# Kernel tuning notes

Measured on AMD Instinct MI355X. Metric: run time of the kernel, lower is better.

## Reference

```python
import jax, jax.numpy as jnp
import numpy as np

N_DET, N_MAP, N_PTS, C = 900, 100, 20, 256
IMG_W, IMG_H = 640.0, 480.0


def _grid_sample(feat, gx, gy):
    """Bilinear grid_sample, align_corners=False, zeros padding.
    feat: [C,H,W]; gx,gy: [N] normalized in [-1,1]. Returns [N,C]."""
    Cc, H, W = feat.shape
    x = (gx + 1.0) * (W * 0.5) - 0.5
    y = (gy + 1.0) * (H * 0.5) - 0.5
    x0 = jnp.floor(x); y0 = jnp.floor(y)
    wx1 = x - x0; wx0 = 1.0 - wx1
    wy1 = y - y0; wy0 = 1.0 - wy1

    def gather(xi, yi):
        inb = (xi >= 0) & (xi <= W - 1) & (yi >= 0) & (yi <= H - 1)
        xc = jnp.clip(xi, 0, W - 1).astype(jnp.int32)
        yc = jnp.clip(yi, 0, H - 1).astype(jnp.int32)
        return feat[:, yc, xc] * inb.astype(feat.dtype)  # [C,N]

    out = (gather(x0, y0) * (wx0 * wy0) + gather(x0 + 1, y0) * (wx1 * wy0)
           + gather(x0, y0 + 1) * (wx0 * wy1) + gather(x0 + 1, y0 + 1) * (wx1 * wy1))
    return out.T  # [N,C]


def _project(E, K, homo):
    """E:[6,4,4], K:[6,3,3], homo:[N,4] -> gx,gy,valid each [6,N]."""
    pc = jnp.einsum('cij,nj->cni', E, homo)            # [6,N,4]
    p2d = jnp.einsum('cij,cnj->cni', K, pc[..., :3])   # [6,N,3]
    depth = p2d[..., 2]
    u = p2d[..., 0] / (depth + 1e-6)
    v = p2d[..., 1] / (depth + 1e-6)
    valid = depth > 0.1
    gx = u / IMG_W * 2.0 - 1.0
    gy = v / IMG_H * 2.0 - 1.0
    return gx, gy, valid


def _sample_multiscale(feats, gx, gy, valid):
    """feats: list of [6,C,H,W]; gx,gy,valid: [6,N] -> [6,N,C]."""
    acc = None
    for f in feats:  # fixed 4 FPN levels
        s = jax.vmap(_grid_sample)(f, gx, gy)  # [6,N,C]
        acc = s if acc is None else acc + s
    acc = acc / len(feats)
    return acc * valid[..., None].astype(acc.dtype)


def setup_inputs():
    key = jax.random.key(0)
    ks = jax.random.split(key, 16)
    f = lambda i, shape, s=1.0: jax.random.normal(ks[i], shape, jnp.float32) * s
    p2 = f(0, (6, C, 120, 160))
    p3 = f(1, (6, C, 60, 80))
    p4 = f(2, (6, C, 30, 40))
    p5 = f(3, (6, C, 15, 20))
    K0 = jnp.array([[500.0, 0.0, 320.0], [0.0, 500.0, 240.0], [0.0, 0.0, 1.0]], jnp.float32)
    intrinsics = jnp.tile(K0, (6, 1, 1)) + f(4, (6, 3, 3), 0.5)
    extrinsics = jnp.tile(jnp.eye(4, dtype=jnp.float32), (6, 1, 1)) + f(5, (6, 4, 4), 0.3)
    det_anchors_3d = f(6, (N_DET, 3), 20.0)
    det_anchors_full = f(7, (N_DET, 11))
    map_anchors = f(8, (N_MAP, N_PTS, 2), 20.0)
    s = 1.0 / float(np.sqrt(C))
    return {
        'p2': p2, 'p3': p3, 'p4': p4, 'p5': p5,
        'intrinsics': intrinsics, 'extrinsics': extrinsics,
        'det_anchors_3d': det_anchors_3d, 'det_anchors_full': det_anchors_full,
        'map_anchors': map_anchors,
        'W1d': f(9, (C, C), s), 'b1d': jnp.zeros((C,), jnp.float32),
        'Wcd': f(10, (C, 4), s), 'bcd': jnp.zeros((4,), jnp.float32),
        'Wod': f(11, (C, 11), s), 'bod': jnp.zeros((11,), jnp.float32),
        'W1m': f(12, (C, C), s), 'b1m': jnp.zeros((C,), jnp.float32),
        'Wcm': f(13, (C, 3), s), 'bcm': jnp.zeros((3,), jnp.float32),
        'Wom': f(14, (C, N_PTS * 2), s), 'bom': jnp.zeros((N_PTS * 2,), jnp.float32),
    }


def reference(p2, p3, p4, p5, intrinsics, extrinsics, det_anchors_3d,
              det_anchors_full, map_anchors, W1d, b1d, Wcd, bcd, Wod, bod,
              W1m, b1m, Wcm, bcm, Wom, bom):
    feats = [p2, p3, p4, p5]
    ones_det = jnp.ones((N_DET, 1), det_anchors_3d.dtype)
    homo_det = jnp.concatenate([det_anchors_3d, ones_det], axis=-1)  # [900,4]
    centers = map_anchors.mean(axis=1)  # [100,2]
    homo_map = jnp.concatenate([centers,
                                jnp.zeros((N_MAP, 1), centers.dtype),
                                jnp.ones((N_MAP, 1), centers.dtype)], axis=-1)  # [100,4]

    gxd, gyd, vd = _project(extrinsics, intrinsics, homo_det)
    det_agg = _sample_multiscale(feats, gxd, gyd, vd).sum(0) / 6.0  # [900,256]
    gxm, gym, vm = _project(extrinsics, intrinsics, homo_map)
    map_agg = _sample_multiscale(feats, gxm, gym, vm).sum(0) / 6.0  # [100,256]

    hd = jax.nn.relu(det_agg @ W1d + b1d)
    det_classes = hd @ Wcd + bcd                     # [900,4]
    det_boxes = det_anchors_full + hd @ Wod + bod    # [900,11]
    hm = jax.nn.relu(map_agg @ W1m + b1m)
    map_classes = hm @ Wcm + bcm                     # [100,3]
    map_lines = map_anchors + (hm @ Wom + bom).reshape(N_MAP, N_PTS, 2)
    return det_classes, det_boxes, map_classes, map_lines
```

## Files before the change

kernel.cpp:

```cpp
#include <hip/hip_runtime.h>

#define CDIM 256
#define NDET 900
#define NMAP 100
#define NPTS 20
#define NBLK (NDET + NMAP)

using u16 = unsigned short;

#define U4OFF 7372800
#define U5OFF 9216000
#define ACC6F 4838400
#define C3STR 1228800
#define C4STR 307200
#define C5STR 76800

__device__ __forceinline__ u16 f2bf(float f) {
    union { float f; unsigned int i; } v; v.f = f;
    return (u16)((v.i + 0x7FFFu + ((v.i >> 16) & 1u)) >> 16);
}
__device__ __forceinline__ float bf2f(u16 u) {
    union { unsigned int i; float f; } v; v.i = ((unsigned int)u) << 16; return v.f;
}

__global__ __launch_bounds__(256, 4) void k1_pack_p2(
    const float* __restrict__ p2, const float* __restrict__ p3,
    const float* __restrict__ p4, const float* __restrict__ p5,
    const float* __restrict__ Kin, const float* __restrict__ Ein,
    const float* __restrict__ det3d, const float* __restrict__ mapanch,
    u16* __restrict__ wsb, float* __restrict__ acc6)
{
    const int b = blockIdx.x;
    const int t = threadIdx.x;

    __shared__ float s_tile[64][65];

    if (b < 1800) {
        const int cam = b / 300;
        const int rem = b % 300;
        const int pxT = rem >> 2, chT = rem & 3;
        const int lane = t & 63, wv = t >> 6;
        #pragma unroll
        for (int cc = 0; cc < 16; ++cc) {
            const int chl = wv * 16 + cc;
            s_tile[chl][lane] = p3[(cam * CDIM + chT * 64 + chl) * 4800 + pxT * 64 + lane];
        }
        __syncthreads();
        #pragma unroll
        for (int pp = 0; pp < 16; ++pp) {
            const int pxl = wv * 16 + pp;
            wsb[(cam * 4800 + pxT * 64 + pxl) * CDIM + chT * 64 + lane] = f2bf(s_tile[lane][pxl]);
        }
        return;
    }
    if (b < 1980) {
        const int id = b - 1800;
        const int cam = id / 30, h = id % 30;
        const float4* __restrict__ src = (const float4*)(p4 + ((cam * CDIM + t) * 30 + h) * 40);
        u16* __restrict__ dst = wsb + U4OFF + ((cam * 30 + h) * 40) * CDIM + t;
        #pragma unroll
        for (int w4 = 0; w4 < 10; ++w4) {
            const float4 v = src[w4];
            dst[(w4 * 4 + 0) * CDIM] = f2bf(v.x);
            dst[(w4 * 4 + 1) * CDIM] = f2bf(v.y);
            dst[(w4 * 4 + 2) * CDIM] = f2bf(v.z);
            dst[(w4 * 4 + 3) * CDIM] = f2bf(v.w);
        }
        return;
    }
    if (b < 2070) {
        const int id = b - 1980;
        const int cam = id / 15, h = id % 15;
        const float4* __restrict__ src = (const float4*)(p5 + ((cam * CDIM + t) * 15 + h) * 20);
        u16* __restrict__ dst = wsb + U5OFF + ((cam * 15 + h) * 20) * CDIM + t;
        #pragma unroll
        for (int w4 = 0; w4 < 5; ++w4) {
            const float4 v = src[w4];
            dst[(w4 * 4 + 0) * CDIM] = f2bf(v.x);
            dst[(w4 * 4 + 1) * CDIM] = f2bf(v.y);
            dst[(w4 * 4 + 2) * CDIM] = f2bf(v.z);
            dst[(w4 * 4 + 3) * CDIM] = f2bf(v.w);
        }
        return;
    }

    const int id = b - 2070;
    const int cam = id / 1000;
    const int pt = id % 1000;
    const bool isDet = (pt < NDET);
    const int m = pt - NDET;

    float h0, h1, h2;
    if (isDet) {
        h0 = det3d[pt * 3 + 0];
        h1 = det3d[pt * 3 + 1];
        h2 = det3d[pt * 3 + 2];
    } else {
        float cx = 0.f, cy = 0.f;
        #pragma unroll
        for (int j = 0; j < NPTS; ++j) {
            cx += mapanch[(m * NPTS + j) * 2 + 0];
            cy += mapanch[(m * NPTS + j) * 2 + 1];
        }
        h0 = cx / (float)NPTS; h1 = cy / (float)NPTS; h2 = 0.f;
    }
    float pc[3];
    #pragma unroll
    for (int i = 0; i < 3; ++i) {
        pc[i] = Ein[cam * 16 + i * 4 + 0] * h0
              + Ein[cam * 16 + i * 4 + 1] * h1
              + Ein[cam * 16 + i * 4 + 2] * h2
              + Ein[cam * 16 + i * 4 + 3] * 1.f;
    }
    const float q0 = Kin[cam*9+0]*pc[0] + Kin[cam*9+1]*pc[1] + Kin[cam*9+2]*pc[2];
    const float q1 = Kin[cam*9+3]*pc[0] + Kin[cam*9+4]*pc[1] + Kin[cam*9+5]*pc[2];
    const float q2 = Kin[cam*9+6]*pc[0] + Kin[cam*9+7]*pc[1] + Kin[cam*9+8]*pc[2];
    const float depth = q2;
    const float u = q0 / (depth + 1e-6f);
    const float v = q1 / (depth + 1e-6f);
    const bool valid = (depth > 0.1f);
    const float gx = u / 640.0f * 2.0f - 1.0f;
    const float gy = v / 480.0f * 2.0f - 1.0f;
    const int H = 120, W = 160;
    const float x = (gx + 1.f) * (W * 0.5f) - 0.5f;
    const float y = (gy + 1.f) * (H * 0.5f) - 0.5f;
    const float x0f = floorf(x), y0f = floorf(y);
    const float wx1 = x - x0f, wx0 = 1.f - wx1;
    const float wy1 = y - y0f, wy0 = 1.f - wy1;
    const float x1f = x0f + 1.f, y1f = y0f + 1.f;
    const bool bx0 = (x0f >= 0.f) && (x0f <= (float)(W - 1));
    const bool bx1 = (x1f >= 0.f) && (x1f <= (float)(W - 1));
    const bool by0 = (y0f >= 0.f) && (y0f <= (float)(H - 1));
    const bool by1 = (y1f >= 0.f) && (y1f <= (float)(H - 1));
    const int xc0 = (int)fminf(fmaxf(x0f, 0.f), (float)(W - 1));
    const int xc1 = (int)fminf(fmaxf(x1f, 0.f), (float)(W - 1));
    const int yc0 = (int)fminf(fmaxf(y0f, 0.f), (float)(H - 1));
    const int yc1 = (int)fminf(fmaxf(y1f, 0.f), (float)(H - 1));
    const float w0 = (bx0 && by0) ? wx0 * wy0 : 0.f;
    const float w1 = (bx1 && by0) ? wx1 * wy0 : 0.f;
    const float w2 = (bx0 && by1) ? wx0 * wy1 : 0.f;
    const float w3 = (bx1 && by1) ? wx1 * wy1 : 0.f;

    float res = 0.f;
    if (valid && ((w0 + w1 + w2 + w3) != 0.f)) {
        const int base = cam * CDIM * H * W + t * (H * W);
        const float v0 = p2[base + yc0 * W + xc0];
        const float v1 = p2[base + yc0 * W + xc1];
        const float v2 = p2[base + yc1 * W + xc0];
        const float v3 = p2[base + yc1 * W + xc1];
        res = w0 * v0 + w1 * v1 + w2 * v2 + w3 * v3;
    }
    acc6[(cam * 1000 + pt) * CDIM + t] = res;
}

__global__ __launch_bounds__(256, 4) void k2_gather_mlp(
    const u16* __restrict__ wsb, const float* __restrict__ acc6,
    const float* __restrict__ Kin, const float* __restrict__ Ein,
    const float* __restrict__ det3d, const float* __restrict__ detfull,
    const float* __restrict__ mapanch,
    const float* __restrict__ W1d, const float* __restrict__ b1d,
    const float* __restrict__ Wcd, const float* __restrict__ bcd,
    const float* __restrict__ Wod, const float* __restrict__ bod,
    const float* __restrict__ W1m, const float* __restrict__ b1m,
    const float* __restrict__ Wcm, const float* __restrict__ bcm,
    const float* __restrict__ Wom, const float* __restrict__ bom,
    float* __restrict__ out)
{
    const int pt = blockIdx.x;
    const int t  = threadIdx.x;
    const bool isDet = (pt < NDET);
    const int m = pt - NDET;

    __shared__ int   s_off[19][4];
    __shared__ float s_w[19][4];
    __shared__ int   s_list[24];
    __shared__ int   s_n;
    __shared__ float s_vec[CDIM];
    __shared__ float s_hid[CDIM];

    float a0 = acc6[(0 * 1000 + pt) * CDIM + t];
    float a1 = acc6[(1 * 1000 + pt) * CDIM + t];
    float a2 = acc6[(2 * 1000 + pt) * CDIM + t];
    float a3 = acc6[(3 * 1000 + pt) * CDIM + t];
    float a4 = acc6[(4 * 1000 + pt) * CDIM + t];
    float a5 = acc6[(5 * 1000 + pt) * CDIM + t];
    float acc = ((((a0 + a1) + a2) + a3) + a4) + a5;

    if (t < 19) {
        float h0, h1, h2;
        if (isDet) {
            h0 = det3d[pt * 3 + 0];
            h1 = det3d[pt * 3 + 1];
            h2 = det3d[pt * 3 + 2];
        } else {
            float cx = 0.f, cy = 0.f;
            #pragma unroll
            for (int j = 0; j < NPTS; ++j) {
                cx += mapanch[(m * NPTS + j) * 2 + 0];
                cy += mapanch[(m * NPTS + j) * 2 + 1];
            }
            h0 = cx / (float)NPTS; h1 = cy / (float)NPTS; h2 = 0.f;
        }
        bool pred = false;
        if (t < 18) {
            const int cam = t / 3, l = 1 + (t % 3);
            float pc[3];
            #pragma unroll
            for (int i = 0; i < 3; ++i) {
                pc[i] = Ein[cam * 16 + i * 4 + 0] * h0
                      + Ein[cam * 16 + i * 4 + 1] * h1
                      + Ein[cam * 16 + i * 4 + 2] * h2
                      + Ein[cam * 16 + i * 4 + 3] * 1.f;
            }
            const float q0 = Kin[cam*9+0]*pc[0] + Kin[cam*9+1]*pc[1] + Kin[cam*9+2]*pc[2];
            const float q1 = Kin[cam*9+3]*pc[0] + Kin[cam*9+4]*pc[1] + Kin[cam*9+5]*pc[2];
            const float q2 = Kin[cam*9+6]*pc[0] + Kin[cam*9+7]*pc[1] + Kin[cam*9+8]*pc[2];
            const float depth = q2;
            const float u = q0 / (depth + 1e-6f);
            const float v = q1 / (depth + 1e-6f);
            const bool valid = (depth > 0.1f);
            const float gx = u / 640.0f * 2.0f - 1.0f;
            const float gy = v / 480.0f * 2.0f - 1.0f;
            const int Hs[4] = {120, 60, 30, 15};
            const int Ws[4] = {160, 80, 40, 20};
            const int H = Hs[l], W = Ws[l];
            const float x = (gx + 1.f) * (W * 0.5f) - 0.5f;
            const float y = (gy + 1.f) * (H * 0.5f) - 0.5f;
            const float x0f = floorf(x), y0f = floorf(y);
            const float wx1 = x - x0f, wx0 = 1.f - wx1;
            const float wy1 = y - y0f, wy0 = 1.f - wy1;
            const float x1f = x0f + 1.f, y1f = y0f + 1.f;
            const bool bx0 = (x0f >= 0.f) && (x0f <= (float)(W - 1));
            const bool bx1 = (x1f >= 0.f) && (x1f <= (float)(W - 1));
            const bool by0 = (y0f >= 0.f) && (y0f <= (float)(H - 1));
            const bool by1 = (y1f >= 0.f) && (y1f <= (float)(H - 1));
            const int xc0 = (int)fminf(fmaxf(x0f, 0.f), (float)(W - 1));
            const int xc1 = (int)fminf(fmaxf(x1f, 0.f), (float)(W - 1));
            const int yc0 = (int)fminf(fmaxf(y0f, 0.f), (float)(H - 1));
            const int yc1 = (int)fminf(fmaxf(y1f, 0.f), (float)(H - 1));
            const int pb = (l == 1) ? cam * C3STR
                         : (l == 2) ? (U4OFF + cam * C4STR)
                                    : (U5OFF + cam * C5STR);
            s_off[t][0] = pb + (yc0 * W + xc0) * CDIM;
            s_off[t][1] = pb + (yc0 * W + xc1) * CDIM;
            s_off[t][2] = pb + (yc1 * W + xc0) * CDIM;
            s_off[t][3] = pb + (yc1 * W + xc1) * CDIM;
            const float w0 = (bx0 && by0) ? wx0 * wy0 : 0.f;
            const float w1 = (bx1 && by0) ? wx1 * wy0 : 0.f;
            const float w2 = (bx0 && by1) ? wx0 * wy1 : 0.f;
            const float w3 = (bx1 && by1) ? wx1 * wy1 : 0.f;
            s_w[t][0] = w0; s_w[t][1] = w1; s_w[t][2] = w2; s_w[t][3] = w3;
            pred = valid && ((w0 + w1 + w2 + w3) != 0.f);
        } else {
            s_off[18][0] = 0; s_off[18][1] = 0; s_off[18][2] = 0; s_off[18][3] = 0;
            s_w[18][0] = 0.f; s_w[18][1] = 0.f; s_w[18][2] = 0.f; s_w[18][3] = 0.f;
        }
        const unsigned long long mask = __ballot(pred);
        const int n = __popcll(mask);
        const int rank = __popcll(mask & ((1ull << t) - 1ull));
        if (pred) s_list[rank] = t;
        const int npad = (n + 7) & ~7;
        if (t < 8 && (n + t) < npad) s_list[n + t] = 18;
        if (t == 0) s_n = npad;
    }
    __syncthreads();

    const int npad = s_n;
    for (int base = 0; base < npad; base += 8) {
        float v[8][4];
        int tj[8];
        #pragma unroll
        for (int j = 0; j < 8; ++j) {
            const int tt = s_list[base + j];
            tj[j] = tt;
            v[j][0] = bf2f(wsb[s_off[tt][0] + t]);
            v[j][1] = bf2f(wsb[s_off[tt][1] + t]);
            v[j][2] = bf2f(wsb[s_off[tt][2] + t]);
            v[j][3] = bf2f(wsb[s_off[tt][3] + t]);
        }
        #pragma unroll
        for (int j = 0; j < 8; ++j) {
            const int tt = tj[j];
            acc += s_w[tt][0] * v[j][0] + s_w[tt][1] * v[j][1]
                 + s_w[tt][2] * v[j][2] + s_w[tt][3] * v[j][3];
        }
    }
    const float agg = (acc * 0.25f) / 6.0f;

    s_vec[t] = agg;
    __syncthreads();

    const float* __restrict__ W1 = isDet ? W1d : W1m;
    const float* __restrict__ b1 = isDet ? b1d : b1m;
    float hsum = b1[t];
    const float4* sv4 = (const float4*)s_vec;
    float wvA[32], wvB[32];
    #pragma unroll
    for (int i = 0; i < 32; ++i) wvA[i] = W1[i * CDIM + t];
    #pragma unroll
    for (int k0 = 0; k0 < CDIM; k0 += 64) {
        #pragma unroll
        for (int i = 0; i < 32; ++i) wvB[i] = W1[(k0 + 32 + i) * CDIM + t];
        #pragma unroll
        for (int i = 0; i < 8; ++i) {
            const float4 x = sv4[(k0 >> 2) + i];
            hsum = fmaf(x.x, wvA[4 * i + 0], hsum);
            hsum = fmaf(x.y, wvA[4 * i + 1], hsum);
            hsum = fmaf(x.z, wvA[4 * i + 2], hsum);
            hsum = fmaf(x.w, wvA[4 * i + 3], hsum);
        }
        if (k0 + 64 < CDIM) {
            #pragma unroll
            for (int i = 0; i < 32; ++i) wvA[i] = W1[(k0 + 64 + i) * CDIM + t];
        }
        #pragma unroll
        for (int i = 0; i < 8; ++i) {
            const float4 x = sv4[(k0 >> 2) + 8 + i];
            hsum = fmaf(x.x, wvB[4 * i + 0], hsum);
            hsum = fmaf(x.y, wvB[4 * i + 1], hsum);
            hsum = fmaf(x.z, wvB[4 * i + 2], hsum);
            hsum = fmaf(x.w, wvB[4 * i + 3], hsum);
        }
    }
    s_hid[t] = fmaxf(hsum, 0.f);
    __syncthreads();

    const int g  = t >> 4;
    const int ln = t & 15;
    const int nOut = isDet ? 15 : 43;
    const int nrep = isDet ? 1 : 3;
    for (int rep = 0; rep < nrep; ++rep) {
        const int o = g + rep * 16;
        if (o < nOut) {
            const float* Wp; int stride, oo, ooff; float bias;
            if (isDet) {
                if (o < 4) { Wp = Wcd; stride = 4;  oo = o;     ooff = pt * 4 + oo;         bias = bcd[oo]; }
                else       { Wp = Wod; stride = 11; oo = o - 4; ooff = 3600 + pt * 11 + oo; bias = bod[oo] + detfull[pt * 11 + oo]; }
            } else {
                if (o < 3) { Wp = Wcm; stride = 3;  oo = o;     ooff = 13500 + m * 3 + oo;  bias = bcm[oo]; }
                else       { Wp = Wom; stride = 40; oo = o - 3; ooff = 13800 + m * 40 + oo; bias = bom[oo] + mapanch[m * 40 + oo]; }
            }
            float wv[16], xv[16];
            #pragma unroll
            for (int kk = 0; kk < 16; ++kk) wv[kk] = Wp[(ln + kk * 16) * stride + oo];
            #pragma unroll
            for (int kk = 0; kk < 16; ++kk) xv[kk] = s_hid[ln + kk * 16];
            float sp = 0.f;
            #pragma unroll
            for (int kk = 0; kk < 16; ++kk) sp = fmaf(xv[kk], wv[kk], sp);
            #pragma unroll
            for (int off = 1; off < 16; off <<= 1) sp += __shfl_xor(sp, off, 64);
            if (ln == 0) out[ooff] = sp + bias;
        }
    }
}

extern "C" void kernel_launch(void* const* d_in, const int* in_sizes, int n_in,
                              void* d_out, int out_size, void* d_ws, size_t ws_size,
                              hipStream_t stream) {
    const float* p2      = (const float*)d_in[0];
    const float* p3      = (const float*)d_in[1];
    const float* p4      = (const float*)d_in[2];
    const float* p5      = (const float*)d_in[3];
    const float* Kin     = (const float*)d_in[4];
    const float* Ein     = (const float*)d_in[5];
    const float* det3d   = (const float*)d_in[6];
    const float* detfull = (const float*)d_in[7];
    const float* mapanch = (const float*)d_in[8];
    const float* W1d     = (const float*)d_in[9];
    const float* b1d     = (const float*)d_in[10];
    const float* Wcd     = (const float*)d_in[11];
    const float* bcd     = (const float*)d_in[12];
    const float* Wod     = (const float*)d_in[13];
    const float* bod     = (const float*)d_in[14];
    const float* W1m     = (const float*)d_in[15];
    const float* b1m     = (const float*)d_in[16];
    const float* Wcm     = (const float*)d_in[17];
    const float* bcm     = (const float*)d_in[18];
    const float* Wom     = (const float*)d_in[19];
    const float* bom     = (const float*)d_in[20];
    float* out = (float*)d_out;
    u16* wsb = (u16*)d_ws;
    float* acc6 = (float*)d_ws + ACC6F;

    k1_pack_p2<<<8070, 256, 0, stream>>>(
        p2, p3, p4, p5, Kin, Ein, det3d, mapanch, wsb, acc6);

    k2_gather_mlp<<<NBLK, 256, 0, stream>>>(
        wsb, acc6, Kin, Ein, det3d, detfull, mapanch,
        W1d, b1d, Wcd, bcd, Wod, bod, W1m, b1m, Wcm, bcm, Wom, bom, out);
}
```

Baseline: 44.54 us.

## Interleave pack and gather blocks, transpose p4/p5 via shared-memory tiles

Repartitions the first kernel's grid so each group of 349 blocks holds 99 pack blocks and 250 gather blocks. Pack (memory-bound transpose) and p2 gather work then run concurrently across the device instead of in separate phases. The p4/p5 bf16 packing moves from per-thread strided stores to the same 64x64 shared-memory tiled transpose used for p3, so writes coalesce. This adds some bounds-check divergence on partial tiles and more pack blocks.

```diff
diff --git a/kernel.cpp b/kernel.cpp
--- a/kernel.cpp
+++ b/kernel.cpp
@@ -14,6 +14,11 @@
 #define C3STR 1228800
 #define C4STR 307200
 #define C5STR 76800
+
+#define NPACK 2376
+#define NGATH 6000
+#define GRP   349
+#define NGRPS 24
 
 __device__ __forceinline__ u16 f2bf(float f) {
     union { float f; unsigned int i; } v; v.f = f;
@@ -35,58 +40,75 @@
 
     __shared__ float s_tile[64][65];
 
-    if (b < 1800) {
-        const int cam = b / 300;
-        const int rem = b % 300;
-        const int pxT = rem >> 2, chT = rem & 3;
+    const int grp = b / GRP, r = b % GRP;
+    const bool isPack = (r < 99);
+    if (isPack) {
+        const int pid = grp * 99 + r;
         const int lane = t & 63, wv = t >> 6;
-        #pragma unroll
-        for (int cc = 0; cc < 16; ++cc) {
-            const int chl = wv * 16 + cc;
-            s_tile[chl][lane] = p3[(cam * CDIM + chT * 64 + chl) * 4800 + pxT * 64 + lane];
-        }
-        __syncthreads();
-        #pragma unroll
-        for (int pp = 0; pp < 16; ++pp) {
-            const int pxl = wv * 16 + pp;
-            wsb[(cam * 4800 + pxT * 64 + pxl) * CDIM + chT * 64 + lane] = f2bf(s_tile[lane][pxl]);
+        if (pid < 1800) {
+            const int cam = pid / 300;
+            const int rem = pid % 300;
+            const int pxT = rem >> 2, chT = rem & 3;
+            #pragma unroll
+            for (int cc = 0; cc < 16; ++cc) {
+                const int chl = wv * 16 + cc;
+                s_tile[chl][lane] = p3[(cam * CDIM + chT * 64 + chl) * 4800 + pxT * 64 + lane];
+            }
+            __syncthreads();
+            #pragma unroll
+            for (int pp = 0; pp < 16; ++pp) {
+                const int pxl = wv * 16 + pp;
+                wsb[(cam * 4800 + pxT * 64 + pxl) * CDIM + chT * 64 + lane] = f2bf(s_tile[lane][pxl]);
+            }
+        } else if (pid < 2256) {
+            const int id = pid - 1800;
+            const int cam = id / 76;
+            const int rem = id % 76;
+            const int pxT = rem >> 2, chT = rem & 3;
+            const int px0 = pxT * 64;
+            #pragma unroll
+            for (int cc = 0; cc < 16; ++cc) {
+                const int chl = wv * 16 + cc;
+                const int px = px0 + lane;
+                s_tile[chl][lane] = (px < 1200)
+                    ? p4[(cam * CDIM + chT * 64 + chl) * 1200 + px] : 0.f;
+            }
+            __syncthreads();
+            #pragma unroll
+            for (int pp = 0; pp < 16; ++pp) {
+                const int pxl = wv * 16 + pp;
+                const int px = px0 + pxl;
+                if (px < 1200)
+                    wsb[U4OFF + (cam * 1200 + px) * CDIM + chT * 64 + lane] = f2bf(s_tile[lane][pxl]);
+            }
+        } else {
+            const int id = pid - 2256;
+            const int cam = id / 20;
+            const int rem = id % 20;
+            const int pxT = rem >> 2, chT = rem & 3;
+            const int px0 = pxT * 64;
+            #pragma unroll
+            for (int cc = 0; cc < 16; ++cc) {
+                const int chl = wv * 16 + cc;
+                const int px = px0 + lane;
+                s_tile[chl][lane] = (px < 300)
+                    ? p5[(cam * CDIM + chT * 64 + chl) * 300 + px] : 0.f;
+            }
+            __syncthreads();
+            #pragma unroll
+            for (int pp = 0; pp < 16; ++pp) {
+                const int pxl = wv * 16 + pp;
+                const int px = px0 + pxl;
+                if (px < 300)
+                    wsb[U5OFF + (cam * 300 + px) * CDIM + chT * 64 + lane] = f2bf(s_tile[lane][pxl]);
+            }
         }
         return;
     }
-    if (b < 1980) {
-        const int id = b - 1800;
-        const int cam = id / 30, h = id % 30;
-        const float4* __restrict__ src = (const float4*)(p4 + ((cam * CDIM + t) * 30 + h) * 40);
-        u16* __restrict__ dst = wsb + U4OFF + ((cam * 30 + h) * 40) * CDIM + t;
-        #pragma unroll
-        for (int w4 = 0; w4 < 10; ++w4) {
-            const float4 v = src[w4];
-            dst[(w4 * 4 + 0) * CDIM] = f2bf(v.x);
-            dst[(w4 * 4 + 1) * CDIM] = f2bf(v.y);
-            dst[(w4 * 4 + 2) * CDIM] = f2bf(v.z);
-            dst[(w4 * 4 + 3) * CDIM] = f2bf(v.w);
-        }
-        return;
-    }
-    if (b < 2070) {
-        const int id = b - 1980;
-        const int cam = id / 15, h = id % 15;
-        const float4* __restrict__ src = (const float4*)(p5 + ((cam * CDIM + t) * 15 + h) * 20);
-        u16* __restrict__ dst = wsb + U5OFF + ((cam * 15 + h) * 20) * CDIM + t;
-        #pragma unroll
-        for (int w4 = 0; w4 < 5; ++w4) {
-            const float4 v = src[w4];
-            dst[(w4 * 4 + 0) * CDIM] = f2bf(v.x);
-            dst[(w4 * 4 + 1) * CDIM] = f2bf(v.y);
-            dst[(w4 * 4 + 2) * CDIM] = f2bf(v.z);
-            dst[(w4 * 4 + 3) * CDIM] = f2bf(v.w);
-        }
-        return;
-    }
-
-    const int id = b - 2070;
-    const int cam = id / 1000;
-    const int pt = id % 1000;
+
+    const int gid = grp * 250 + (r - 99);
+    const int cam = gid / 1000;
+    const int pt  = gid % 1000;
     const bool isDet = (pt < NDET);
     const int m = pt - NDET;
 
@@ -143,7 +165,7 @@
 
     float res = 0.f;
     if (valid && ((w0 + w1 + w2 + w3) != 0.f)) {
-        const int base = cam * CDIM * H * W + t * (H * W);
+        const int base = (cam * CDIM + t) * (H * W);
         const float v0 = p2[base + yc0 * W + xc0];
         const float v1 = p2[base + yc0 * W + xc1];
         const float v2 = p2[base + yc1 * W + xc0];
@@ -178,12 +200,12 @@
     __shared__ float s_vec[CDIM];
     __shared__ float s_hid[CDIM];
 
-    float a0 = acc6[(0 * 1000 + pt) * CDIM + t];
-    float a1 = acc6[(1 * 1000 + pt) * CDIM + t];
-    float a2 = acc6[(2 * 1000 + pt) * CDIM + t];
-    float a3 = acc6[(3 * 1000 + pt) * CDIM + t];
-    float a4 = acc6[(4 * 1000 + pt) * CDIM + t];
-    float a5 = acc6[(5 * 1000 + pt) * CDIM + t];
+    const float a0 = acc6[(0 * 1000 + pt) * CDIM + t];
+    const float a1 = acc6[(1 * 1000 + pt) * CDIM + t];
+    const float a2 = acc6[(2 * 1000 + pt) * CDIM + t];
+    const float a3 = acc6[(3 * 1000 + pt) * CDIM + t];
+    const float a4 = acc6[(4 * 1000 + pt) * CDIM + t];
+    const float a5 = acc6[(5 * 1000 + pt) * CDIM + t];
     float acc = ((((a0 + a1) + a2) + a3) + a4) + a5;
 
     if (t < 19) {
@@ -383,7 +405,7 @@
     u16* wsb = (u16*)d_ws;
     float* acc6 = (float*)d_ws + ACC6F;
 
-    k1_pack_p2<<<8070, 256, 0, stream>>>(
+    k1_pack_p2<<<NPACK + NGATH, 256, 0, stream>>>(
         p2, p3, p4, p5, Kin, Ein, det3d, mapanch, wsb, acc6);
 
     k2_gather_mlp<<<NBLK, 256, 0, stream>>>(
```

After: 46.62 us. 1.05x slower.

## Process two points per block in gather-MLP and store p2 partials as bf16

Applied to the files above, without the earlier changes.

The gather+MLP kernel now handles two points per block (500 blocks instead of 1000), so each W1 weight row loaded into registers is reused for two hidden vectors, and the output-head weights are reused too. The per-camera p2 partial sums are stored as bf16 rather than fp32, halving that workspace's write and read traffic. In exchange there are fewer blocks to spread across CUs, more register pressure, and some precision loss on the p2 contribution.

```diff
diff --git a/kernel.cpp b/kernel.cpp
--- a/kernel.cpp
+++ b/kernel.cpp
@@ -4,13 +4,12 @@
 #define NDET 900
 #define NMAP 100
 #define NPTS 20
-#define NBLK (NDET + NMAP)
 
 using u16 = unsigned short;
 
 #define U4OFF 7372800
 #define U5OFF 9216000
-#define ACC6F 4838400
+#define UEND  9292800
 #define C3STR 1228800
 #define C4STR 307200
 #define C5STR 76800
@@ -28,7 +27,7 @@
     const float* __restrict__ p4, const float* __restrict__ p5,
     const float* __restrict__ Kin, const float* __restrict__ Ein,
     const float* __restrict__ det3d, const float* __restrict__ mapanch,
-    u16* __restrict__ wsb, float* __restrict__ acc6)
+    u16* __restrict__ wsb, u16* __restrict__ accb)
 {
     const int b = blockIdx.x;
     const int t = threadIdx.x;
@@ -143,18 +142,18 @@
 
     float res = 0.f;
     if (valid && ((w0 + w1 + w2 + w3) != 0.f)) {
-        const int base = cam * CDIM * H * W + t * (H * W);
+        const int base = (cam * CDIM + t) * (H * W);
         const float v0 = p2[base + yc0 * W + xc0];
         const float v1 = p2[base + yc0 * W + xc1];
         const float v2 = p2[base + yc1 * W + xc0];
         const float v3 = p2[base + yc1 * W + xc1];
         res = w0 * v0 + w1 * v1 + w2 * v2 + w3 * v3;
     }
-    acc6[(cam * 1000 + pt) * CDIM + t] = res;
+    accb[(cam * 1000 + pt) * CDIM + t] = f2bf(res);
 }
 
 __global__ __launch_bounds__(256, 4) void k2_gather_mlp(
-    const u16* __restrict__ wsb, const float* __restrict__ acc6,
+    const u16* __restrict__ wsb, const u16* __restrict__ accb,
     const float* __restrict__ Kin, const float* __restrict__ Ein,
     const float* __restrict__ det3d, const float* __restrict__ detfull,
     const float* __restrict__ mapanch,
@@ -166,134 +165,141 @@
     const float* __restrict__ Wom, const float* __restrict__ bom,
     float* __restrict__ out)
 {
-    const int pt = blockIdx.x;
-    const int t  = threadIdx.x;
-    const bool isDet = (pt < NDET);
-    const int m = pt - NDET;
-
-    __shared__ int   s_off[19][4];
-    __shared__ float s_w[19][4];
-    __shared__ int   s_list[24];
-    __shared__ int   s_n;
-    __shared__ float s_vec[CDIM];
-    __shared__ float s_hid[CDIM];
-
-    float a0 = acc6[(0 * 1000 + pt) * CDIM + t];
-    float a1 = acc6[(1 * 1000 + pt) * CDIM + t];
-    float a2 = acc6[(2 * 1000 + pt) * CDIM + t];
-    float a3 = acc6[(3 * 1000 + pt) * CDIM + t];
-    float a4 = acc6[(4 * 1000 + pt) * CDIM + t];
-    float a5 = acc6[(5 * 1000 + pt) * CDIM + t];
-    float acc = ((((a0 + a1) + a2) + a3) + a4) + a5;
-
-    if (t < 19) {
-        float h0, h1, h2;
-        if (isDet) {
-            h0 = det3d[pt * 3 + 0];
-            h1 = det3d[pt * 3 + 1];
-            h2 = det3d[pt * 3 + 2];
-        } else {
-            float cx = 0.f, cy = 0.f;
+    const int b = blockIdx.x;
+    const int t = threadIdx.x;
+    const bool isDet = (b < 450);
+    const int pt0 = isDet ? (b * 2) : (NDET + (b - 450) * 2);
+
+    __shared__ int   s_off[2][19][4];
+    __shared__ float s_w[2][19][4];
+    __shared__ int   s_list[2][24];
+    __shared__ int   s_n[2];
+    __shared__ float s_vec[2][CDIM];
+    __shared__ float s_hid[2][CDIM];
+
+    #pragma unroll
+    for (int p = 0; p < 2; ++p) {
+        const int pt = pt0 + p;
+        const int m = pt - NDET;
+        if (t < 19) {
+            float h0, h1, h2;
+            if (isDet) {
+                h0 = det3d[pt * 3 + 0];
+                h1 = det3d[pt * 3 + 1];
+                h2 = det3d[pt * 3 + 2];
+            } else {
+                float cx = 0.f, cy = 0.f;
+                #pragma unroll
+                for (int j = 0; j < NPTS; ++j) {
+                    cx += mapanch[(m * NPTS + j) * 2 + 0];
+                    cy += mapanch[(m * NPTS + j) * 2 + 1];
+                }
+                h0 = cx / (float)NPTS; h1 = cy / (float)NPTS; h2 = 0.f;
+            }
+            bool pred = false;
+            if (t < 18) {
+                const int cam = t / 3, l = 1 + (t % 3);
+                float pc[3];
+                #pragma unroll
+                for (int i = 0; i < 3; ++i) {
+                    pc[i] = Ein[cam * 16 + i * 4 + 0] * h0
+                          + Ein[cam * 16 + i * 4 + 1] * h1
+                          + Ein[cam * 16 + i * 4 + 2] * h2
+                          + Ein[cam * 16 + i * 4 + 3] * 1.f;
+                }
+                const float q0 = Kin[cam*9+0]*pc[0] + Kin[cam*9+1]*pc[1] + Kin[cam*9+2]*pc[2];
+                const float q1 = Kin[cam*9+3]*pc[0] + Kin[cam*9+4]*pc[1] + Kin[cam*9+5]*pc[2];
+                const float q2 = Kin[cam*9+6]*pc[0] + Kin[cam*9+7]*pc[1] + Kin[cam*9+8]*pc[2];
+                const float depth = q2;
+                const float u = q0 / (depth + 1e-6f);
+                const float v = q1 / (depth + 1e-6f);
+                const bool valid = (depth > 0.1f);
+                const float gx = u / 640.0f * 2.0f - 1.0f;
+                const float gy = v / 480.0f * 2.0f - 1.0f;
+                const int Hs[4] = {120, 60, 30, 15};
+                const int Ws[4] = {160, 80, 40, 20};
+                const int H = Hs[l], W = Ws[l];
+                const float x = (gx + 1.f) * (W * 0.5f) - 0.5f;
+                const float y = (gy + 1.f) * (H * 0.5f) - 0.5f;
+                const float x0f = floorf(x), y0f = floorf(y);
+                const float wx1 = x - x0f, wx0 = 1.f - wx1;
+                const float wy1 = y - y0f, wy0 = 1.f - wy1;
+                const float x1f = x0f + 1.f, y1f = y0f + 1.f;
+                const bool bx0 = (x0f >= 0.f) && (x0f <= (float)(W - 1));
+                const bool bx1 = (x1f >= 0.f) && (x1f <= (float)(W - 1));
+                const bool by0 = (y0f >= 0.f) && (y0f <= (float)(H - 1));
+                const bool by1 = (y1f >= 0.f) && (y1f <= (float)(H - 1));
+                const int xc0 = (int)fminf(fmaxf(x0f, 0.f), (float)(W - 1));
+                const int xc1 = (int)fminf(fmaxf(x1f, 0.f), (float)(W - 1));
+                const int yc0 = (int)fminf(fmaxf(y0f, 0.f), (float)(H - 1));
+                const int yc1 = (int)fminf(fmaxf(y1f, 0.f), (float)(H - 1));
+                const int pb = (l == 1) ? cam * C3STR
+                             : (l == 2) ? (U4OFF + cam * C4STR)
+                                        : (U5OFF + cam * C5STR);
+                s_off[p][t][0] = pb + (yc0 * W + xc0) * CDIM;
+                s_off[p][t][1] = pb + (yc0 * W + xc1) * CDIM;
+                s_off[p][t][2] = pb + (yc1 * W + xc0) * CDIM;
+                s_off[p][t][3] = pb + (yc1 * W + xc1) * CDIM;
+                const float w0 = (bx0 && by0) ? wx0 * wy0 : 0.f;
+                const float w1 = (bx1 && by0) ? wx1 * wy0 : 0.f;
+                const float w2 = (bx0 && by1) ? wx0 * wy1 : 0.f;
+                const float w3 = (bx1 && by1) ? wx1 * wy1 : 0.f;
+                s_w[p][t][0] = w0; s_w[p][t][1] = w1; s_w[p][t][2] = w2; s_w[p][t][3] = w3;
+                pred = valid && ((w0 + w1 + w2 + w3) != 0.f);
+            } else {
+                s_off[p][18][0] = 0; s_off[p][18][1] = 0; s_off[p][18][2] = 0; s_off[p][18][3] = 0;
+                s_w[p][18][0] = 0.f; s_w[p][18][1] = 0.f; s_w[p][18][2] = 0.f; s_w[p][18][3] = 0.f;
+            }
+            const unsigned long long mask = __ballot(pred);
+            const int n = __popcll(mask);
+            const int rank = __popcll(mask & ((1ull << t) - 1ull));
+            if (pred) s_list[p][rank] = t;
+            const int npad = (n + 7) & ~7;
+            if (t < 8 && (n + t) < npad) s_list[p][n + t] = 18;
+            if (t == 0) s_n[p] = npad;
+        }
+    }
+    __syncthreads();
+
+    #pragma unroll
+    for (int p = 0; p < 2; ++p) {
+        const int pt = pt0 + p;
+        float acc = bf2f(accb[(0 * 1000 + pt) * CDIM + t]);
+        acc += bf2f(accb[(1 * 1000 + pt) * CDIM + t]);
+        acc += bf2f(accb[(2 * 1000 + pt) * CDIM + t]);
+        acc += bf2f(accb[(3 * 1000 + pt) * CDIM + t]);
+        acc += bf2f(accb[(4 * 1000 + pt) * CDIM + t]);
+        acc += bf2f(accb[(5 * 1000 + pt) * CDIM + t]);
+
+        const int npad = s_n[p];
+        for (int base = 0; base < npad; base += 8) {
+            float v[8][4];
+            int tj[8];
             #pragma unroll
-            for (int j = 0; j < NPTS; ++j) {
-                cx += mapanch[(m * NPTS + j) * 2 + 0];
-                cy += mapanch[(m * NPTS + j) * 2 + 1];
-            }
-            h0 = cx / (float)NPTS; h1 = cy / (float)NPTS; h2 = 0.f;
-        }
-        bool pred = false;
-        if (t < 18) {
-            const int cam = t / 3, l = 1 + (t % 3);
-            float pc[3];
+            for (int j = 0; j < 8; ++j) {
+                const int tt = s_list[p][base + j];
+                tj[j] = tt;
+                v[j][0] = bf2f(wsb[s_off[p][tt][0] + t]);
+                v[j][1] = bf2f(wsb[s_off[p][tt][1] + t]);
+                v[j][2] = bf2f(wsb[s_off[p][tt][2] + t]);
+                v[j][3] = bf2f(wsb[s_off[p][tt][3] + t]);
+            }
             #pragma unroll
-            for (int i = 0; i < 3; ++i) {
-                pc[i] = Ein[cam * 16 + i * 4 + 0] * h0
-                      + Ein[cam * 16 + i * 4 + 1] * h1
-                      + Ein[cam * 16 + i * 4 + 2] * h2
-                      + Ein[cam * 16 + i * 4 + 3] * 1.f;
-            }
-            const float q0 = Kin[cam*9+0]*pc[0] + Kin[cam*9+1]*pc[1] + Kin[cam*9+2]*pc[2];
-            const float q1 = Kin[cam*9+3]*pc[0] + Kin[cam*9+4]*pc[1] + Kin[cam*9+5]*pc[2];
-            const float q2 = Kin[cam*9+6]*pc[0] + Kin[cam*9+7]*pc[1] + Kin[cam*9+8]*pc[2];
-            const float depth = q2;
-            const float u = q0 / (depth + 1e-6f);
-            const float v = q1 / (depth + 1e-6f);
-            const bool valid = (depth > 0.1f);
-            const float gx = u / 640.0f * 2.0f - 1.0f;
-            const float gy = v / 480.0f * 2.0f - 1.0f;
-            const int Hs[4] = {120, 60, 30, 15};
-            const int Ws[4] = {160, 80, 40, 20};
-            const int H = Hs[l], W = Ws[l];
-            const float x = (gx + 1.f) * (W * 0.5f) - 0.5f;
-            const float y = (gy + 1.f) * (H * 0.5f) - 0.5f;
-            const float x0f = floorf(x), y0f = floorf(y);
-            const float wx1 = x - x0f, wx0 = 1.f - wx1;
-            const float wy1 = y - y0f, wy0 = 1.f - wy1;
-            const float x1f = x0f + 1.f, y1f = y0f + 1.f;
-            const bool bx0 = (x0f >= 0.f) && (x0f <= (float)(W - 1));
-            const bool bx1 = (x1f >= 0.f) && (x1f <= (float)(W - 1));
-            const bool by0 = (y0f >= 0.f) && (y0f <= (float)(H - 1));
-            const bool by1 = (y1f >= 0.f) && (y1f <= (float)(H - 1));
-            const int xc0 = (int)fminf(fmaxf(x0f, 0.f), (float)(W - 1));
-            const int xc1 = (int)fminf(fmaxf(x1f, 0.f), (float)(W - 1));
-            const int yc0 = (int)fminf(fmaxf(y0f, 0.f), (float)(H - 1));
-            const int yc1 = (int)fminf(fmaxf(y1f, 0.f), (float)(H - 1));
-            const int pb = (l == 1) ? cam * C3STR
-                         : (l == 2) ? (U4OFF + cam * C4STR)
-                                    : (U5OFF + cam * C5STR);
-            s_off[t][0] = pb + (yc0 * W + xc0) * CDIM;
-            s_off[t][1] = pb + (yc0 * W + xc1) * CDIM;
-            s_off[t][2] = pb + (yc1 * W + xc0) * CDIM;
-            s_off[t][3] = pb + (yc1 * W + xc1) * CDIM;
-            const float w0 = (bx0 && by0) ? wx0 * wy0 : 0.f;
-            const float w1 = (bx1 && by0) ? wx1 * wy0 : 0.f;
-            const float w2 = (bx0 && by1) ? wx0 * wy1 : 0.f;
-            const float w3 = (bx1 && by1) ? wx1 * wy1 : 0.f;
-            s_w[t][0] = w0; s_w[t][1] = w1; s_w[t][2] = w2; s_w[t][3] = w3;
-            pred = valid && ((w0 + w1 + w2 + w3) != 0.f);
-        } else {
-            s_off[18][0] = 0; s_off[18][1] = 0; s_off[18][2] = 0; s_off[18][3] = 0;
-            s_w[18][0] = 0.f; s_w[18][1] = 0.f; s_w[18][2] = 0.f; s_w[18][3] = 0.f;
-        }
-        const unsigned long long mask = __ballot(pred);
-        const int n = __popcll(mask);
-        const int rank = __popcll(mask & ((1ull << t) - 1ull));
-        if (pred) s_list[rank] = t;
-        const int npad = (n + 7) & ~7;
-        if (t < 8 && (n + t) < npad) s_list[n + t] = 18;
-        if (t == 0) s_n = npad;
+            for (int j = 0; j < 8; ++j) {
+                const int tt = tj[j];
+                acc += s_w[p][tt][0] * v[j][0] + s_w[p][tt][1] * v[j][1]
+                     + s_w[p][tt][2] * v[j][2] + s_w[p][tt][3] * v[j][3];
+            }
+        }
+        s_vec[p][t] = (acc * 0.25f) / 6.0f;
     }
     __syncthreads();
 
-    const int npad = s_n;
-    for (int base = 0; base < npad; base += 8) {
-        float v[8][4];
-        int tj[8];
-        #pragma unroll
-        for (int j = 0; j < 8; ++j) {
-            const int tt = s_list[base + j];
-            tj[j] = tt;
-            v[j][0] = bf2f(wsb[s_off[tt][0] + t]);
-            v[j][1] = bf2f(wsb[s_off[tt][1] + t]);
-            v[j][2] = bf2f(wsb[s_off[tt][2] + t]);
-            v[j][3] = bf2f(wsb[s_off[tt][3] + t]);
-        }
-        #pragma unroll
-        for (int j = 0; j < 8; ++j) {
-            const int tt = tj[j];
-            acc += s_w[tt][0] * v[j][0] + s_w[tt][1] * v[j][1]
-                 + s_w[tt][2] * v[j][2] + s_w[tt][3] * v[j][3];
-        }
-    }
-    const float agg = (acc * 0.25f) / 6.0f;
-
-    s_vec[t] = agg;
-    __syncthreads();
-
     const float* __restrict__ W1 = isDet ? W1d : W1m;
-    const float* __restrict__ b1 = isDet ? b1d : b1m;
-    float hsum = b1[t];
-    const float4* sv4 = (const float4*)s_vec;
+    const float bb = (isDet ? b1d : b1m)[t];
+    float hs0 = bb, hs1 = bb;
+    const float4* sv0 = (const float4*)s_vec[0];
+    const float4* sv1 = (const float4*)s_vec[1];
     float wvA[32], wvB[32];
     #pragma unroll
     for (int i = 0; i < 32; ++i) wvA[i] = W1[i * CDIM + t];
@@ -303,11 +309,12 @@
         for (int i = 0; i < 32; ++i) wvB[i] = W1[(k0 + 32 + i) * CDIM + t];
         #pragma unroll
         for (int i = 0; i < 8; ++i) {
-            const float4 x = sv4[(k0 >> 2) + i];
-            hsum = fmaf(x.x, wvA[4 * i + 0], hsum);
-            hsum = fmaf(x.y, wvA[4 * i + 1], hsum);
-            hsum = fmaf(x.z, wvA[4 * i + 2], hsum);
-            hsum = fmaf(x.w, wvA[4 * i + 3], hsum);
+            const float4 x0 = sv0[(k0 >> 2) + i];
+            const float4 x1 = sv1[(k0 >> 2) + i];
+            hs0 = fmaf(x0.x, wvA[4*i+0], hs0); hs1 = fmaf(x1.x, wvA[4*i+0], hs1);
+            hs0 = fmaf(x0.y, wvA[4*i+1], hs0); hs1 = fmaf(x1.y, wvA[4*i+1], hs1);
+            hs0 = fmaf(x0.z, wvA[4*i+2], hs0); hs1 = fmaf(x1.z, wvA[4*i+2], hs1);
+            hs0 = fmaf(x0.w, wvA[4*i+3], hs0); hs1 = fmaf(x1.w, wvA[4*i+3], hs1);
         }
         if (k0 + 64 < CDIM) {
             #pragma unroll
@@ -315,14 +322,16 @@
         }
         #pragma unroll
         for (int i = 0; i < 8; ++i) {
-            const float4 x = sv4[(k0 >> 2) + 8 + i];
-            hsum = fmaf(x.x, wvB[4 * i + 0], hsum);
-            hsum = fmaf(x.y, wvB[4 * i + 1], hsum);
-            hsum = fmaf(x.z, wvB[4 * i + 2], hsum);
-            hsum = fmaf(x.w, wvB[4 * i + 3], hsum);
-        }
-    }
-    s_hid[t] = fmaxf(hsum, 0.f);
+            const float4 x0 = sv0[(k0 >> 2) + 8 + i];
+            const float4 x1 = sv1[(k0 >> 2) + 8 + i];
+            hs0 = fmaf(x0.x, wvB[4*i+0], hs0); hs1 = fmaf(x1.x, wvB[4*i+0], hs1);
+            hs0 = fmaf(x0.y, wvB[4*i+1], hs0); hs1 = fmaf(x1.y, wvB[4*i+1], hs1);
+            hs0 = fmaf(x0.z, wvB[4*i+2], hs0); hs1 = fmaf(x1.z, wvB[4*i+2], hs1);
+            hs0 = fmaf(x0.w, wvB[4*i+3], hs0); hs1 = fmaf(x1.w, wvB[4*i+3], hs1);
+        }
+    }
+    s_hid[0][t] = fmaxf(hs0, 0.f);
+    s_hid[1][t] = fmaxf(hs1, 0.f);
     __syncthreads();
 
     const int g  = t >> 4;
@@ -332,25 +341,40 @@
     for (int rep = 0; rep < nrep; ++rep) {
         const int o = g + rep * 16;
         if (o < nOut) {
-            const float* Wp; int stride, oo, ooff; float bias;
+            const float* Wp; int stride, oo;
             if (isDet) {
-                if (o < 4) { Wp = Wcd; stride = 4;  oo = o;     ooff = pt * 4 + oo;         bias = bcd[oo]; }
-                else       { Wp = Wod; stride = 11; oo = o - 4; ooff = 3600 + pt * 11 + oo; bias = bod[oo] + detfull[pt * 11 + oo]; }
+                if (o < 4) { Wp = Wcd; stride = 4;  oo = o; }
+                else       { Wp = Wod; stride = 11; oo = o - 4; }
             } else {
-                if (o < 3) { Wp = Wcm; stride = 3;  oo = o;     ooff = 13500 + m * 3 + oo;  bias = bcm[oo]; }
-                else       { Wp = Wom; stride = 40; oo = o - 3; ooff = 13800 + m * 40 + oo; bias = bom[oo] + mapanch[m * 40 + oo]; }
-            }
-            float wv[16], xv[16];
+                if (o < 3) { Wp = Wcm; stride = 3;  oo = o; }
+                else       { Wp = Wom; stride = 40; oo = o - 3; }
+            }
+            float wv[16];
             #pragma unroll
             for (int kk = 0; kk < 16; ++kk) wv[kk] = Wp[(ln + kk * 16) * stride + oo];
             #pragma unroll
-            for (int kk = 0; kk < 16; ++kk) xv[kk] = s_hid[ln + kk * 16];
-            float sp = 0.f;
-            #pragma unroll
-            for (int kk = 0; kk < 16; ++kk) sp = fmaf(xv[kk], wv[kk], sp);
-            #pragma unroll
-            for (int off = 1; off < 16; off <<= 1) sp += __shfl_xor(sp, off, 64);
-            if (ln == 0) out[ooff] = sp + bias;
+            for (int p = 0; p < 2; ++p) {
+                float sp = 0.f;
+                #pragma unroll
+                for (int kk = 0; kk < 16; ++kk) {
+                    sp = fmaf(s_hid[p][ln + kk * 16], wv[kk], sp);
+                }
+                #pragma unroll
+                for (int off = 1; off < 16; off <<= 1) sp += __shfl_xor(sp, off, 64);
+                if (ln == 0) {
+                    const int pt = pt0 + p;
+                    const int m = pt - NDET;
+                    float bias; int ooff;
+                    if (isDet) {
+                        if (o < 4) { bias = bcd[oo];                         ooff = pt * 4 + oo; }
+                        else       { bias = bod[oo] + detfull[pt * 11 + oo]; ooff = 3600 + pt * 11 + oo; }
+                    } else {
+                        if (o < 3) { bias = bcm[oo];                         ooff = 13500 + m * 3 + oo; }
+                        else       { bias = bom[oo] + mapanch[m * 40 + oo];  ooff = 13800 + m * 40 + oo; }
+                    }
+                    out[ooff] = sp + bias;
+                }
+            }
         }
     }
 }
@@ -380,13 +404,13 @@
     const float* Wom     = (const float*)d_in[19];
     const float* bom     = (const float*)d_in[20];
     float* out = (float*)d_out;
-    u16* wsb = (u16*)d_ws;
-    float* acc6 = (float*)d_ws + ACC6F;
+    u16* wsb  = (u16*)d_ws;
+    u16* accb = wsb + UEND;
 
     k1_pack_p2<<<8070, 256, 0, stream>>>(
-        p2, p3, p4, p5, Kin, Ein, det3d, mapanch, wsb, acc6);
-
-    k2_gather_mlp<<<NBLK, 256, 0, stream>>>(
-        wsb, acc6, Kin, Ein, det3d, detfull, mapanch,
+        p2, p3, p4, p5, Kin, Ein, det3d, mapanch, wsb, accb);
+
+    k2_gather_mlp<<<500, 256, 0, stream>>>(
+        wsb, accb, Kin, Ein, det3d, detfull, mapanch,
         W1d, b1d, Wcd, bcd, Wod, bod, W1m, b1m, Wcm, bcm, Wom, bom, out);
 }
```

Result: faster. 43.11 us, median of 2 (-3.2%).
